# Performance work log

Measured on AMD Instinct MI355X. Metric: run time of the kernel, lower is better.

Reference implementation:

```python
import jax, jax.numpy as jnp
import numpy as np

B, S, H, QIN, RIN = 32, 8192, 256, 256, 256
TANH_EXPLORATION = 10.0


def setup_inputs() -> dict:
    key = jax.random.key(0)
    ks = jax.random.split(key, 7)
    bound = 1.0 / np.sqrt(H)
    return {
        "query": jax.random.normal(ks[0], (B, QIN), dtype=jnp.float32),
        "ref": jax.random.normal(ks[1], (S, B, RIN), dtype=jnp.float32),
        # nn.Linear(QIN, H): weight [H, QIN], bias [H]
        "Wq": jax.random.normal(ks[2], (H, QIN), dtype=jnp.float32) * (1.0 / np.sqrt(QIN)),
        "bq": jax.random.normal(ks[3], (H,), dtype=jnp.float32) * 0.01,
        # nn.Conv1d(RIN, H, kernel=1): equivalent to a pointwise linear, weight [H, RIN], bias [H]
        "Wr": jax.random.normal(ks[4], (H, RIN), dtype=jnp.float32) * (1.0 / np.sqrt(RIN)),
        "br": jax.random.normal(ks[5], (H,), dtype=jnp.float32) * 0.01,
        "v": jax.random.uniform(ks[6], (H,), dtype=jnp.float32, minval=-bound, maxval=bound),
    }


def reference(query, ref, Wq, bq, Wr, br, v):
    # ref: [S, B, RIN] -> permute(1,2,0) -> [B, RIN, S]
    ref_p = jnp.transpose(ref, (1, 2, 0))
    # project_query: [B, H]
    q = query @ Wq.T + bq
    # project_ref (1x1 conv == pointwise linear over channel dim): e [B, H, S]
    e = jnp.einsum("hr,brs->bhs", Wr, ref_p) + br[None, :, None]
    # u[b,s] = sum_h v[h] * tanh(q[b,h] + e[b,h,s])
    u = jnp.einsum("h,bhs->bs", v, jnp.tanh(q[:, :, None] + e))
    # use_tanh=True path
    return e, TANH_EXPLORATION * jnp.tanh(u)
```

## Files before the change

### kernel.cpp

```cpp
#include <hip/hip_runtime.h>

#define NB 32
#define NS 8192
#define NH 256
#define NR 256
#define NQ 256

typedef __bf16 bf16x8 __attribute__((ext_vector_type(8)));
typedef float  f32x4  __attribute__((ext_vector_type(4)));

__device__ __forceinline__ float fast_tanh(float x) {
  x = fminf(15.0f, fmaxf(-15.0f, x));
  float e = __expf(2.0f * x);
  return (e - 1.0f) * __builtin_amdgcn_rcpf(e + 1.0f);
}

__device__ __forceinline__ void split8(float4 a, float4 b, bf16x8& hi, bf16x8& lo) {
  float x[8] = {a.x, a.y, a.z, a.w, b.x, b.y, b.z, b.w};
#pragma unroll
  for (int j = 0; j < 8; ++j) {
    __bf16 h = (__bf16)x[j];
    hi[j] = h;
    lo[j] = (__bf16)(x[j] - (float)h);
  }
}

__global__ __launch_bounds__(256) void prep_kernel(
    const float* __restrict__ query, const float* __restrict__ Wq,
    const float* __restrict__ bq, const float* __restrict__ Wr,
    float* __restrict__ ws_q, __bf16* __restrict__ wsAhi, __bf16* __restrict__ wsAlo) {
  const int tid = threadIdx.x;
  const int blk = blockIdx.x;
  if (blk < NB) {
    const float4* qr = reinterpret_cast<const float4*>(query + blk * NQ);
    const float4* wr = reinterpret_cast<const float4*>(Wq + tid * NQ);
    float acc = 0.0f;
#pragma unroll 8
    for (int i = 0; i < NQ / 4; ++i) {
      float4 a = qr[i], w = wr[i];
      acc += a.x * w.x + a.y * w.y + a.z * w.z + a.w * w.w;
    }
    ws_q[blk * NH + tid] = acc + bq[tid];
  } else {
    const int gid = (blk - NB) * 256 + tid;
    const int l  = gid & 63;
    const int mt = (gid >> 6) & 15;
    const int ks = gid >> 10;
    const int row = 16 * mt + (l & 15);
    const int kb  = 32 * ks + 8 * (l >> 4);
    const float4* src = reinterpret_cast<const float4*>(Wr + row * NR + kb);
    bf16x8 hi, lo;
    split8(src[0], src[1], hi, lo);
    *reinterpret_cast<bf16x8*>(wsAhi + (size_t)gid * 8) = hi;
    *reinterpret_cast<bf16x8*>(wsAlo + (size_t)gid * 8) = lo;
  }
}

__global__ __launch_bounds__(256, 2) void attn_kernel(
    const float* __restrict__ ref, const float* __restrict__ br,
    const float* __restrict__ v, const float* __restrict__ ws_q,
    const __bf16* __restrict__ wsAhi, const __bf16* __restrict__ wsAlo,
    float* __restrict__ e_out, float* __restrict__ u_out) {
  __shared__ __bf16 lXhi[4 * 64 * 8];
  __shared__ __bf16 lXlo[4 * 64 * 8];
  __shared__ float  u_part[4][64];

  const int tid = threadIdx.x;
  const int l   = tid & 63;
  const int wm  = tid >> 6;
  const int s0  = blockIdx.x * 64;
  const int b   = blockIdx.y;

  const float* srcX = ref + (size_t)(s0 + 16 * wm + (l & 15)) * (NB * NR)
                          + (size_t)b * NR + 8 * (l >> 4);

  f32x4 acc[4][4];
  const f32x4 zero = {0.f, 0.f, 0.f, 0.f};
#pragma unroll
  for (int mt = 0; mt < 4; ++mt)
#pragma unroll
    for (int nt = 0; nt < 4; ++nt) acc[mt][nt] = zero;

#pragma unroll 1
  for (int ks = 0; ks < NR / 32; ++ks) {
    bf16x8 ah[4], al[4];
#pragma unroll
    for (int mt = 0; mt < 4; ++mt) {
      const size_t fo = ((size_t)(ks * 16 + wm * 4 + mt) * 64 + l) * 8;
      ah[mt] = *reinterpret_cast<const bf16x8*>(wsAhi + fo);
      al[mt] = *reinterpret_cast<const bf16x8*>(wsAlo + fo);
    }
    __syncthreads();
    float4 x0 = *reinterpret_cast<const float4*>(srcX + ks * 32);
    float4 x1 = *reinterpret_cast<const float4*>(srcX + ks * 32 + 4);
    bf16x8 xhi, xlo;
    split8(x0, x1, xhi, xlo);
    *reinterpret_cast<bf16x8*>(lXhi + tid * 8) = xhi;
    *reinterpret_cast<bf16x8*>(lXlo + tid * 8) = xlo;
    __syncthreads();

    bf16x8 bh[4], bl[4];
#pragma unroll
    for (int nt = 0; nt < 4; ++nt) {
      bh[nt] = *reinterpret_cast<const bf16x8*>(lXhi + (nt * 64 + l) * 8);
      bl[nt] = *reinterpret_cast<const bf16x8*>(lXlo + (nt * 64 + l) * 8);
    }
#pragma unroll
    for (int mt = 0; mt < 4; ++mt) {
#pragma unroll
      for (int nt = 0; nt < 4; ++nt) {
        acc[mt][nt] = __builtin_amdgcn_mfma_f32_16x16x32_bf16(ah[mt], bh[nt], acc[mt][nt], 0, 0, 0);
        acc[mt][nt] = __builtin_amdgcn_mfma_f32_16x16x32_bf16(ah[mt], bl[nt], acc[mt][nt], 0, 0, 0);
        acc[mt][nt] = __builtin_amdgcn_mfma_f32_16x16x32_bf16(al[mt], bh[nt], acc[mt][nt], 0, 0, 0);
      }
    }
  }

  const int col = l & 15;
  const int rq  = l >> 4;
  float psum[4] = {0.f, 0.f, 0.f, 0.f};
#pragma unroll
  for (int mt = 0; mt < 4; ++mt) {
#pragma unroll
    for (int r = 0; r < 4; ++r) {
      const int h = 64 * wm + 16 * mt + 4 * rq + r;
      const float brv = br[h];
      const float qv  = ws_q[b * NH + h];
      const float vv  = v[h];
#pragma unroll
      for (int nt = 0; nt < 4; ++nt) {
        float e = acc[mt][nt][r] + brv;
        e_out[(size_t)b * NH * NS + (size_t)h * NS + (s0 + 16 * nt + col)] = e;
        psum[nt] += vv * fast_tanh(qv + e);
      }
    }
  }
#pragma unroll
  for (int nt = 0; nt < 4; ++nt) {
    float p = psum[nt];
    p += __shfl_xor(p, 16, 64);
    p += __shfl_xor(p, 32, 64);
    if (l < 16) u_part[wm][16 * nt + col] = p;
  }
  __syncthreads();
  if (tid < 64) {
    float u = u_part[0][tid] + u_part[1][tid] + u_part[2][tid] + u_part[3][tid];
    u_out[(size_t)b * NS + s0 + tid] = 10.0f * fast_tanh(u);
  }
}

extern "C" void kernel_launch(void* const* d_in, const int* in_sizes, int n_in,
                              void* d_out, int out_size, void* d_ws, size_t ws_size,
                              hipStream_t stream) {
  const float* query = (const float*)d_in[0];
  const float* ref   = (const float*)d_in[1];
  const float* Wq    = (const float*)d_in[2];
  const float* bq    = (const float*)d_in[3];
  const float* Wr    = (const float*)d_in[4];
  const float* br    = (const float*)d_in[5];
  const float* v     = (const float*)d_in[6];

  float* e_out = (float*)d_out;
  float* u_out = e_out + (size_t)NB * NH * NS;

  float*  ws_q  = (float*)d_ws;
  __bf16* wsAhi = (__bf16*)((char*)d_ws + 32 * 1024);
  __bf16* wsAlo = (__bf16*)((char*)d_ws + 32 * 1024 + 128 * 1024);

  prep_kernel<<<dim3(NB + 32), 256, 0, stream>>>(query, Wq, bq, Wr, ws_q, wsAhi, wsAlo);
  attn_kernel<<<dim3(NS / 64, NB), 256, 0, stream>>>(ref, br, v, ws_q, wsAhi, wsAlo, e_out, u_out);
}
```

Measured before the change: 177.5 us.

## Halve sequence tile per block, raise occupancy, and prefetch ref before barrier

Shrinks the per-block sequence tile from 64 to 32 columns, so each wave keeps half the accumulators and the launch bound can rise to 4 blocks per CU. Each thread now loads one float4 of ref (split into hi/lo bf16 halves), and that load is issued at the top of the loop before the weight loads and the barrier, to hide global latency. MFMA sections are wrapped in s_setprio. The cost is twice as many blocks, each re-reading the full split Wr fragments, which doubles weight traffic from L2.

```diff
diff --git a/kernel.cpp b/kernel.cpp
--- a/kernel.cpp
+++ b/kernel.cpp
@@ -7,6 +7,7 @@
 #define NQ 256
 
 typedef __bf16 bf16x8 __attribute__((ext_vector_type(8)));
+typedef __bf16 bf16x4 __attribute__((ext_vector_type(4)));
 typedef float  f32x4  __attribute__((ext_vector_type(4)));
 
 __device__ __forceinline__ float fast_tanh(float x) {
@@ -19,6 +20,16 @@
   float x[8] = {a.x, a.y, a.z, a.w, b.x, b.y, b.z, b.w};
 #pragma unroll
   for (int j = 0; j < 8; ++j) {
+    __bf16 h = (__bf16)x[j];
+    hi[j] = h;
+    lo[j] = (__bf16)(x[j] - (float)h);
+  }
+}
+
+__device__ __forceinline__ void split4(float4 a, bf16x4& hi, bf16x4& lo) {
+  float x[4] = {a.x, a.y, a.z, a.w};
+#pragma unroll
+  for (int j = 0; j < 4; ++j) {
     __bf16 h = (__bf16)x[j];
     hi[j] = h;
     lo[j] = (__bf16)(x[j] - (float)h);
@@ -56,33 +67,37 @@
   }
 }
 
-__global__ __launch_bounds__(256, 2) void attn_kernel(
+__global__ __launch_bounds__(256, 4) void attn_kernel(
     const float* __restrict__ ref, const float* __restrict__ br,
     const float* __restrict__ v, const float* __restrict__ ws_q,
     const __bf16* __restrict__ wsAhi, const __bf16* __restrict__ wsAlo,
     float* __restrict__ e_out, float* __restrict__ u_out) {
-  __shared__ __bf16 lXhi[4 * 64 * 8];
-  __shared__ __bf16 lXlo[4 * 64 * 8];
-  __shared__ float  u_part[4][64];
+  __shared__ __bf16 lXhi[2 * 64 * 8];
+  __shared__ __bf16 lXlo[2 * 64 * 8];
+  __shared__ float  u_part[4][32];
 
   const int tid = threadIdx.x;
   const int l   = tid & 63;
   const int wm  = tid >> 6;
-  const int s0  = blockIdx.x * 64;
+  const int s0  = blockIdx.x * 32;
   const int b   = blockIdx.y;
 
-  const float* srcX = ref + (size_t)(s0 + 16 * wm + (l & 15)) * (NB * NR)
-                          + (size_t)b * NR + 8 * (l >> 4);
+  const int nt_s = tid >> 7;
+  const int ls   = (tid >> 1) & 63;
+  const int half = tid & 1;
+  const float* srcX = ref + (size_t)(s0 + 16 * nt_s + (ls & 15)) * (NB * NR)
+                          + (size_t)b * NR + 8 * (ls >> 4) + 4 * half;
 
-  f32x4 acc[4][4];
+  f32x4 acc[4][2];
   const f32x4 zero = {0.f, 0.f, 0.f, 0.f};
 #pragma unroll
   for (int mt = 0; mt < 4; ++mt)
 #pragma unroll
-    for (int nt = 0; nt < 4; ++nt) acc[mt][nt] = zero;
+    for (int nt = 0; nt < 2; ++nt) acc[mt][nt] = zero;
 
 #pragma unroll 1
   for (int ks = 0; ks < NR / 32; ++ks) {
+    float4 x = *reinterpret_cast<const float4*>(srcX + ks * 32);
     bf16x8 ah[4], al[4];
 #pragma unroll
     for (int mt = 0; mt < 4; ++mt) {
@@ -91,34 +106,34 @@
       al[mt] = *reinterpret_cast<const bf16x8*>(wsAlo + fo);
     }
     __syncthreads();
-    float4 x0 = *reinterpret_cast<const float4*>(srcX + ks * 32);
-    float4 x1 = *reinterpret_cast<const float4*>(srcX + ks * 32 + 4);
-    bf16x8 xhi, xlo;
-    split8(x0, x1, xhi, xlo);
-    *reinterpret_cast<bf16x8*>(lXhi + tid * 8) = xhi;
-    *reinterpret_cast<bf16x8*>(lXlo + tid * 8) = xlo;
+    bf16x4 xhi, xlo;
+    split4(x, xhi, xlo);
+    *reinterpret_cast<bf16x4*>(lXhi + tid * 4) = xhi;
+    *reinterpret_cast<bf16x4*>(lXlo + tid * 4) = xlo;
     __syncthreads();
 
-    bf16x8 bh[4], bl[4];
+    bf16x8 bh[2], bl[2];
 #pragma unroll
-    for (int nt = 0; nt < 4; ++nt) {
+    for (int nt = 0; nt < 2; ++nt) {
       bh[nt] = *reinterpret_cast<const bf16x8*>(lXhi + (nt * 64 + l) * 8);
       bl[nt] = *reinterpret_cast<const bf16x8*>(lXlo + (nt * 64 + l) * 8);
     }
+    __builtin_amdgcn_s_setprio(1);
 #pragma unroll
     for (int mt = 0; mt < 4; ++mt) {
 #pragma unroll
-      for (int nt = 0; nt < 4; ++nt) {
+      for (int nt = 0; nt < 2; ++nt) {
         acc[mt][nt] = __builtin_amdgcn_mfma_f32_16x16x32_bf16(ah[mt], bh[nt], acc[mt][nt], 0, 0, 0);
         acc[mt][nt] = __builtin_amdgcn_mfma_f32_16x16x32_bf16(ah[mt], bl[nt], acc[mt][nt], 0, 0, 0);
         acc[mt][nt] = __builtin_amdgcn_mfma_f32_16x16x32_bf16(al[mt], bh[nt], acc[mt][nt], 0, 0, 0);
       }
     }
+    __builtin_amdgcn_s_setprio(0);
   }
 
   const int col = l & 15;
   const int rq  = l >> 4;
-  float psum[4] = {0.f, 0.f, 0.f, 0.f};
+  float psum[2] = {0.f, 0.f};
 #pragma unroll
   for (int mt = 0; mt < 4; ++mt) {
 #pragma unroll
@@ -128,7 +143,7 @@
       const float qv  = ws_q[b * NH + h];
       const float vv  = v[h];
 #pragma unroll
-      for (int nt = 0; nt < 4; ++nt) {
+      for (int nt = 0; nt < 2; ++nt) {
         float e = acc[mt][nt][r] + brv;
         e_out[(size_t)b * NH * NS + (size_t)h * NS + (s0 + 16 * nt + col)] = e;
         psum[nt] += vv * fast_tanh(qv + e);
@@ -136,14 +151,14 @@
     }
   }
 #pragma unroll
-  for (int nt = 0; nt < 4; ++nt) {
+  for (int nt = 0; nt < 2; ++nt) {
     float p = psum[nt];
     p += __shfl_xor(p, 16, 64);
     p += __shfl_xor(p, 32, 64);
     if (l < 16) u_part[wm][16 * nt + col] = p;
   }
   __syncthreads();
-  if (tid < 64) {
+  if (tid < 32) {
     float u = u_part[0][tid] + u_part[1][tid] + u_part[2][tid] + u_part[3][tid];
     u_out[(size_t)b * NS + s0 + tid] = 10.0f * fast_tanh(u);
   }
@@ -168,5 +183,5 @@
   __bf16* wsAlo = (__bf16*)((char*)d_ws + 32 * 1024 + 128 * 1024);
 
   prep_kernel<<<dim3(NB + 32), 256, 0, stream>>>(query, Wq, bq, Wr, ws_q, wsAhi, wsAlo);
-  attn_kernel<<<dim3(NS / 64, NB), 256, 0, stream>>>(ref, br, v, ws_q, wsAhi, wsAlo, e_out, u_out);
+  attn_kernel<<<dim3(NS / 32, NB), 256, 0, stream>>>(ref, br, v, ws_q, wsAhi, wsAlo, e_out, u_out);
 }
```

New measurement: 225.8 us. 1.27x slower.

## Batch ref loads into two halves, swap MFMA operands for vectorized e stores

Applied to the files above, without the earlier changes.

The K loop now loads ref in two halves of four 32-wide k-slices each. Each half is split to bf16 hi/lo and staged in a larger LDS buffer, so only two barrier-separated phases remain instead of eight. The second half's global loads are issued before the first half's MFMAs to overlap their latency. The MFMA operands are swapped so the accumulator rows map along S, which allows float4 stores of e and a shuffle-based reduction of u. Occupancy hint rises to 3 blocks per CU, which adds LDS and register pressure.

```diff
diff --git a/kernel.cpp b/kernel.cpp
--- a/kernel.cpp
+++ b/kernel.cpp
@@ -56,14 +56,14 @@
   }
 }
 
-__global__ __launch_bounds__(256, 2) void attn_kernel(
+__global__ __launch_bounds__(256, 3) void attn_kernel(
     const float* __restrict__ ref, const float* __restrict__ br,
     const float* __restrict__ v, const float* __restrict__ ws_q,
     const __bf16* __restrict__ wsAhi, const __bf16* __restrict__ wsAlo,
     float* __restrict__ e_out, float* __restrict__ u_out) {
-  __shared__ __bf16 lXhi[4 * 64 * 8];
-  __shared__ __bf16 lXlo[4 * 64 * 8];
-  __shared__ float  u_part[4][64];
+  __shared__ __bf16 lXhi[4 * 2048];
+  __shared__ __bf16 lXlo[4 * 2048];
+  __shared__ __align__(16) float u_part[4][64];
 
   const int tid = threadIdx.x;
   const int l   = tid & 63;
@@ -81,71 +81,114 @@
 #pragma unroll
     for (int nt = 0; nt < 4; ++nt) acc[mt][nt] = zero;
 
-#pragma unroll 1
-  for (int ks = 0; ks < NR / 32; ++ks) {
-    bf16x8 ah[4], al[4];
+  float4 xs[8];
+#pragma unroll
+  for (int t = 0; t < 4; ++t) {
+    xs[2 * t]     = *reinterpret_cast<const float4*>(srcX + t * 32);
+    xs[2 * t + 1] = *reinterpret_cast<const float4*>(srcX + t * 32 + 4);
+  }
+#pragma unroll
+  for (int t = 0; t < 4; ++t) {
+    bf16x8 hi, lo;
+    split8(xs[2 * t], xs[2 * t + 1], hi, lo);
+    *reinterpret_cast<bf16x8*>(lXhi + t * 2048 + tid * 8) = hi;
+    *reinterpret_cast<bf16x8*>(lXlo + t * 2048 + tid * 8) = lo;
+  }
+  __syncthreads();
+
+#pragma unroll
+  for (int t = 0; t < 4; ++t) {
+    xs[2 * t]     = *reinterpret_cast<const float4*>(srcX + 128 + t * 32);
+    xs[2 * t + 1] = *reinterpret_cast<const float4*>(srcX + 128 + t * 32 + 4);
+  }
+
+  auto step = [&](int t, int ks) {
+    bf16x8 wh[4], wl[4], xh[4], xl[4];
+#pragma unroll
+    for (int nt = 0; nt < 4; ++nt) {
+      const size_t fo = ((size_t)(ks * 16 + wm * 4 + nt) * 64 + l) * 8;
+      wh[nt] = *reinterpret_cast<const bf16x8*>(wsAhi + fo);
+      wl[nt] = *reinterpret_cast<const bf16x8*>(wsAlo + fo);
+    }
 #pragma unroll
     for (int mt = 0; mt < 4; ++mt) {
-      const size_t fo = ((size_t)(ks * 16 + wm * 4 + mt) * 64 + l) * 8;
-      ah[mt] = *reinterpret_cast<const bf16x8*>(wsAhi + fo);
-      al[mt] = *reinterpret_cast<const bf16x8*>(wsAlo + fo);
-    }
-    __syncthreads();
-    float4 x0 = *reinterpret_cast<const float4*>(srcX + ks * 32);
-    float4 x1 = *reinterpret_cast<const float4*>(srcX + ks * 32 + 4);
-    bf16x8 xhi, xlo;
-    split8(x0, x1, xhi, xlo);
-    *reinterpret_cast<bf16x8*>(lXhi + tid * 8) = xhi;
-    *reinterpret_cast<bf16x8*>(lXlo + tid * 8) = xlo;
-    __syncthreads();
-
-    bf16x8 bh[4], bl[4];
-#pragma unroll
-    for (int nt = 0; nt < 4; ++nt) {
-      bh[nt] = *reinterpret_cast<const bf16x8*>(lXhi + (nt * 64 + l) * 8);
-      bl[nt] = *reinterpret_cast<const bf16x8*>(lXlo + (nt * 64 + l) * 8);
+      xh[mt] = *reinterpret_cast<const bf16x8*>(lXhi + t * 2048 + (mt * 64 + l) * 8);
+      xl[mt] = *reinterpret_cast<const bf16x8*>(lXlo + t * 2048 + (mt * 64 + l) * 8);
     }
 #pragma unroll
     for (int mt = 0; mt < 4; ++mt) {
 #pragma unroll
       for (int nt = 0; nt < 4; ++nt) {
-        acc[mt][nt] = __builtin_amdgcn_mfma_f32_16x16x32_bf16(ah[mt], bh[nt], acc[mt][nt], 0, 0, 0);
-        acc[mt][nt] = __builtin_amdgcn_mfma_f32_16x16x32_bf16(ah[mt], bl[nt], acc[mt][nt], 0, 0, 0);
-        acc[mt][nt] = __builtin_amdgcn_mfma_f32_16x16x32_bf16(al[mt], bh[nt], acc[mt][nt], 0, 0, 0);
+        acc[mt][nt] = __builtin_amdgcn_mfma_f32_16x16x32_bf16(xh[mt], wh[nt], acc[mt][nt], 0, 0, 0);
+        acc[mt][nt] = __builtin_amdgcn_mfma_f32_16x16x32_bf16(xh[mt], wl[nt], acc[mt][nt], 0, 0, 0);
+        acc[mt][nt] = __builtin_amdgcn_mfma_f32_16x16x32_bf16(xl[mt], wh[nt], acc[mt][nt], 0, 0, 0);
       }
     }
-  }
+  };
+
+  step(0, 0); step(1, 1); step(2, 2); step(3, 3);
+  __syncthreads();
+
+#pragma unroll
+  for (int t = 0; t < 4; ++t) {
+    bf16x8 hi, lo;
+    split8(xs[2 * t], xs[2 * t + 1], hi, lo);
+    *reinterpret_cast<bf16x8*>(lXhi + t * 2048 + tid * 8) = hi;
+    *reinterpret_cast<bf16x8*>(lXlo + t * 2048 + tid * 8) = lo;
+  }
+  __syncthreads();
+
+  step(0, 4); step(1, 5); step(2, 6); step(3, 7);
 
   const int col = l & 15;
   const int rq  = l >> 4;
-  float psum[4] = {0.f, 0.f, 0.f, 0.f};
-#pragma unroll
-  for (int mt = 0; mt < 4; ++mt) {
-#pragma unroll
-    for (int r = 0; r < 4; ++r) {
-      const int h = 64 * wm + 16 * mt + 4 * rq + r;
-      const float brv = br[h];
-      const float qv  = ws_q[b * NH + h];
-      const float vv  = v[h];
-#pragma unroll
-      for (int nt = 0; nt < 4; ++nt) {
-        float e = acc[mt][nt][r] + brv;
-        e_out[(size_t)b * NH * NS + (size_t)h * NS + (s0 + 16 * nt + col)] = e;
-        psum[nt] += vv * fast_tanh(qv + e);
-      }
-    }
-  }
+  f32x4 usum[4];
+#pragma unroll
+  for (int mt = 0; mt < 4; ++mt) usum[mt] = zero;
+
 #pragma unroll
   for (int nt = 0; nt < 4; ++nt) {
-    float p = psum[nt];
-    p += __shfl_xor(p, 16, 64);
-    p += __shfl_xor(p, 32, 64);
-    if (l < 16) u_part[wm][16 * nt + col] = p;
-  }
-  __syncthreads();
-  if (tid < 64) {
-    float u = u_part[0][tid] + u_part[1][tid] + u_part[2][tid] + u_part[3][tid];
-    u_out[(size_t)b * NS + s0 + tid] = 10.0f * fast_tanh(u);
+    const int h = 64 * wm + 16 * nt + col;
+    const float brv = br[h];
+    const float qv  = ws_q[b * NH + h];
+    const float vv  = v[h];
+#pragma unroll
+    for (int mt = 0; mt < 4; ++mt) {
+      f32x4 e4 = acc[mt][nt];
+#pragma unroll
+      for (int r = 0; r < 4; ++r) e4[r] += brv;
+      *reinterpret_cast<f32x4*>(e_out + (size_t)b * NH * NS + (size_t)h * NS
+                                + (s0 + 16 * mt + 4 * rq)) = e4;
+#pragma unroll
+      for (int r = 0; r < 4; ++r) usum[mt][r] += vv * fast_tanh(qv + e4[r]);
+    }
+  }
+#pragma unroll
+  for (int off = 1; off < 16; off <<= 1) {
+#pragma unroll
+    for (int mt = 0; mt < 4; ++mt)
+#pragma unroll
+      for (int r = 0; r < 4; ++r)
+        usum[mt][r] += __shfl_xor(usum[mt][r], off, 64);
+  }
+  if (col == 0) {
+#pragma unroll
+    for (int mt = 0; mt < 4; ++mt)
+      *reinterpret_cast<f32x4*>(&u_part[wm][16 * mt + 4 * rq]) = usum[mt];
+  }
+  __syncthreads();
+  if (tid < 16) {
+    f32x4 u = *reinterpret_cast<const f32x4*>(&u_part[0][4 * tid]);
+#pragma unroll
+    for (int w = 1; w < 4; ++w) {
+      f32x4 t2 = *reinterpret_cast<const f32x4*>(&u_part[w][4 * tid]);
+#pragma unroll
+      for (int r = 0; r < 4; ++r) u[r] += t2[r];
+    }
+    f32x4 o;
+#pragma unroll
+    for (int r = 0; r < 4; ++r) o[r] = 10.0f * fast_tanh(u[r]);
+    *reinterpret_cast<f32x4*>(u_out + (size_t)b * NS + s0 + 4 * tid) = o;
   }
 }
 
```

New measurement: 186.4 us. +5.0%, slower.

## Split attention work by h-chunks, load X directly into registers with prefetch

Applied to the files above, without the earlier changes.

Reassigns blocks so each handles a 64-wide h chunk over 256 s positions, with each wave owning its own s columns. The X tile is loaded straight from global memory into registers with a one-step prefetch, which removes the LDS staging and block barriers. Partial u sums over h chunks go to a workspace and are combined in a new small reduction kernel. This trades barrier and LDS cost for 4x redundant ref reads (hopefully served from L2), redundant bf16 splitting, and an extra launch.

```diff
diff --git a/kernel.cpp b/kernel.cpp
--- a/kernel.cpp
+++ b/kernel.cpp
@@ -60,19 +60,18 @@
     const float* __restrict__ ref, const float* __restrict__ br,
     const float* __restrict__ v, const float* __restrict__ ws_q,
     const __bf16* __restrict__ wsAhi, const __bf16* __restrict__ wsAlo,
-    float* __restrict__ e_out, float* __restrict__ u_out) {
-  __shared__ __bf16 lXhi[4 * 64 * 8];
-  __shared__ __bf16 lXlo[4 * 64 * 8];
-  __shared__ float  u_part[4][64];
-
+    float* __restrict__ e_out, float* __restrict__ u_ws) {
   const int tid = threadIdx.x;
   const int l   = tid & 63;
   const int wm  = tid >> 6;
-  const int s0  = blockIdx.x * 64;
+  const int hc  = blockIdx.x & 3;
+  const int sc  = blockIdx.x >> 2;
   const int b   = blockIdx.y;
+  const int sbase = sc * 256 + wm * 64;
 
-  const float* srcX = ref + (size_t)(s0 + 16 * wm + (l & 15)) * (NB * NR)
+  const float* srcX = ref + (size_t)(sbase + (l & 15)) * (NB * NR)
                           + (size_t)b * NR + 8 * (l >> 4);
+  const size_t ntStride = (size_t)16 * NB * NR;
 
   f32x4 acc[4][4];
   const f32x4 zero = {0.f, 0.f, 0.f, 0.f};
@@ -81,30 +80,34 @@
 #pragma unroll
     for (int nt = 0; nt < 4; ++nt) acc[mt][nt] = zero;
 
+  float4 cb[4][2];
+#pragma unroll
+  for (int nt = 0; nt < 4; ++nt) {
+    cb[nt][0] = *reinterpret_cast<const float4*>(srcX + nt * ntStride);
+    cb[nt][1] = *reinterpret_cast<const float4*>(srcX + nt * ntStride + 4);
+  }
+
 #pragma unroll 1
   for (int ks = 0; ks < NR / 32; ++ks) {
+    const int kofs = (ks < NR / 32 - 1) ? (ks + 1) * 32 : ks * 32;
+    float4 nb[4][2];
+#pragma unroll
+    for (int nt = 0; nt < 4; ++nt) {
+      nb[nt][0] = *reinterpret_cast<const float4*>(srcX + nt * ntStride + kofs);
+      nb[nt][1] = *reinterpret_cast<const float4*>(srcX + nt * ntStride + kofs + 4);
+    }
     bf16x8 ah[4], al[4];
 #pragma unroll
     for (int mt = 0; mt < 4; ++mt) {
-      const size_t fo = ((size_t)(ks * 16 + wm * 4 + mt) * 64 + l) * 8;
+      const size_t fo = ((size_t)(ks * 16 + 4 * hc + mt) * 64 + l) * 8;
       ah[mt] = *reinterpret_cast<const bf16x8*>(wsAhi + fo);
       al[mt] = *reinterpret_cast<const bf16x8*>(wsAlo + fo);
     }
-    __syncthreads();
-    float4 x0 = *reinterpret_cast<const float4*>(srcX + ks * 32);
-    float4 x1 = *reinterpret_cast<const float4*>(srcX + ks * 32 + 4);
-    bf16x8 xhi, xlo;
-    split8(x0, x1, xhi, xlo);
-    *reinterpret_cast<bf16x8*>(lXhi + tid * 8) = xhi;
-    *reinterpret_cast<bf16x8*>(lXlo + tid * 8) = xlo;
-    __syncthreads();
-
     bf16x8 bh[4], bl[4];
 #pragma unroll
-    for (int nt = 0; nt < 4; ++nt) {
-      bh[nt] = *reinterpret_cast<const bf16x8*>(lXhi + (nt * 64 + l) * 8);
-      bl[nt] = *reinterpret_cast<const bf16x8*>(lXlo + (nt * 64 + l) * 8);
-    }
+    for (int nt = 0; nt < 4; ++nt) split8(cb[nt][0], cb[nt][1], bh[nt], bl[nt]);
+
+    __builtin_amdgcn_s_setprio(1);
 #pragma unroll
     for (int mt = 0; mt < 4; ++mt) {
 #pragma unroll
@@ -114,6 +117,9 @@
         acc[mt][nt] = __builtin_amdgcn_mfma_f32_16x16x32_bf16(al[mt], bh[nt], acc[mt][nt], 0, 0, 0);
       }
     }
+    __builtin_amdgcn_s_setprio(0);
+#pragma unroll
+    for (int nt = 0; nt < 4; ++nt) { cb[nt][0] = nb[nt][0]; cb[nt][1] = nb[nt][1]; }
   }
 
   const int col = l & 15;
@@ -123,14 +129,14 @@
   for (int mt = 0; mt < 4; ++mt) {
 #pragma unroll
     for (int r = 0; r < 4; ++r) {
-      const int h = 64 * wm + 16 * mt + 4 * rq + r;
+      const int h = 64 * hc + 16 * mt + 4 * rq + r;
       const float brv = br[h];
       const float qv  = ws_q[b * NH + h];
       const float vv  = v[h];
 #pragma unroll
       for (int nt = 0; nt < 4; ++nt) {
         float e = acc[mt][nt][r] + brv;
-        e_out[(size_t)b * NH * NS + (size_t)h * NS + (s0 + 16 * nt + col)] = e;
+        e_out[(size_t)b * NH * NS + (size_t)h * NS + (sbase + 16 * nt + col)] = e;
         psum[nt] += vv * fast_tanh(qv + e);
       }
     }
@@ -140,13 +146,25 @@
     float p = psum[nt];
     p += __shfl_xor(p, 16, 64);
     p += __shfl_xor(p, 32, 64);
-    if (l < 16) u_part[wm][16 * nt + col] = p;
+    if (rq == 0)
+      u_ws[((size_t)hc * NB + b) * NS + sbase + 16 * nt + col] = p;
   }
-  __syncthreads();
-  if (tid < 64) {
-    float u = u_part[0][tid] + u_part[1][tid] + u_part[2][tid] + u_part[3][tid];
-    u_out[(size_t)b * NS + s0 + tid] = 10.0f * fast_tanh(u);
+}
+
+__global__ __launch_bounds__(256) void ured_kernel(
+    const float* __restrict__ u_ws, float* __restrict__ u_out) {
+  const int i4 = blockIdx.x * 256 + threadIdx.x;
+  f32x4 u = *reinterpret_cast<const f32x4*>(u_ws + (size_t)4 * i4);
+#pragma unroll
+  for (int hc = 1; hc < 4; ++hc) {
+    f32x4 t = *reinterpret_cast<const f32x4*>(u_ws + (size_t)hc * NB * NS + 4 * i4);
+#pragma unroll
+    for (int r = 0; r < 4; ++r) u[r] += t[r];
   }
+  f32x4 o;
+#pragma unroll
+  for (int r = 0; r < 4; ++r) o[r] = 10.0f * fast_tanh(u[r]);
+  *reinterpret_cast<f32x4*>(u_out + (size_t)4 * i4) = o;
 }
 
 extern "C" void kernel_launch(void* const* d_in, const int* in_sizes, int n_in,
@@ -166,7 +184,9 @@
   float*  ws_q  = (float*)d_ws;
   __bf16* wsAhi = (__bf16*)((char*)d_ws + 32 * 1024);
   __bf16* wsAlo = (__bf16*)((char*)d_ws + 32 * 1024 + 128 * 1024);
+  float*  u_ws  = (float*)((char*)d_ws + 32 * 1024 + 256 * 1024);
 
   prep_kernel<<<dim3(NB + 32), 256, 0, stream>>>(query, Wq, bq, Wr, ws_q, wsAhi, wsAlo);
-  attn_kernel<<<dim3(NS / 64, NB), 256, 0, stream>>>(ref, br, v, ws_q, wsAhi, wsAlo, e_out, u_out);
+  attn_kernel<<<dim3(4 * (NS / 256), NB), 256, 0, stream>>>(ref, br, v, ws_q, wsAhi, wsAlo, e_out, u_ws);
+  ured_kernel<<<dim3(NB * NS / 1024), 256, 0, stream>>>(u_ws, u_out);
 }
```

New measurement: 273.1 us. +53.8%, slower.
